# Kernel optimization log

Hardware: AMD Instinct MI355X
Metric: run time of the kernel (lower is better)

The kernel has to match this reference:

```python
import jax, jax.numpy as jnp
import numpy as np

B, S, D, H = 8, 2048, 1024, 64


def setup_inputs() -> dict:
    key = jax.random.key(0)
    ks = jax.random.split(key, 9)
    s = 0.02
    return {
        "x": jax.random.normal(ks[0], (B, S, D), jnp.float32),
        "Wq": jax.random.normal(ks[1], (H, D), jnp.float32) * s,
        "bq": jnp.zeros((H,), jnp.float32),
        "Wk": jax.random.normal(ks[2], (H, D), jnp.float32) * s,
        "bk": jnp.zeros((H,), jnp.float32),
        "Wv": jax.random.normal(ks[3], (H, D), jnp.float32) * s,
        "bv": jnp.zeros((H,), jnp.float32),
        "Wo": jax.random.normal(ks[4], (H, H), jnp.float32) * s,
        "bo": jnp.zeros((H,), jnp.float32),
    }


def reference(x, Wq, bq, Wk, bk, Wv, bv, Wo, bo):
    # Linear layers: y = x @ W.T + b (torch nn.Linear convention)
    q = jnp.einsum("bsd,hd->bsh", x, Wq) + bq  # [B,S,H]
    k = jnp.einsum("bsd,hd->bsh", x, Wk) + bk
    v = jnp.einsum("bsd,hd->bsh", x, Wv) + bv
    scale = jnp.float32(H) ** 0.5
    scores = jnp.einsum("bsh,bth->bst", q, k) / scale  # [B,S,S]
    causal = jnp.tril(jnp.ones((S, S), bool))
    scores = jnp.where(causal, scores, -jnp.inf)
    attn = jax.nn.softmax(scores, axis=-1)
    out = jnp.einsum("bst,bth->bsh", attn, v)  # [B,S,H]
    out = jnp.einsum("bsh,gh->bsg", out, Wo) + bo  # output proj [H,H]
    return out
```

## Files before the change

kernel.cpp:

```cpp
#include <hip/hip_runtime.h>
#include <hip/hip_bf16.h>

#define NB 8
#define NS 2048
#define ND 1024
#define NH 64
#define NM (NB*NS)

typedef __attribute__((ext_vector_type(8))) short short8;
typedef __attribute__((ext_vector_type(4))) short short4v;
typedef __attribute__((ext_vector_type(4))) float f32x4;
typedef __attribute__((ext_vector_type(4))) float f4;

#define QSCALE (0.125f * 1.44269504088896340736f)

__device__ __forceinline__ unsigned short f2bf(float f) {
    union { __hip_bfloat16 h; unsigned short u; } cv;
    cv.h = __float2bfloat16(f);
    return cv.u;
}

__global__ __launch_bounds__(256) void convw_kernel(
    const float* __restrict__ Wq, const float* __restrict__ bq,
    const float* __restrict__ Wk, const float* __restrict__ bk,
    const float* __restrict__ Wv, const float* __restrict__ bv,
    const float* __restrict__ Wo,
    unsigned short* __restrict__ Wb, unsigned short* __restrict__ Wob,
    float* __restrict__ biasb)
{
    const int row = blockIdx.x;
    const int t = threadIdx.x;
    if (row < 192) {
        const float* W = row < 64 ? Wq : (row < 128 ? Wk : Wv);
        const float sc = row < 64 ? QSCALE : 1.0f;
        f4 v = *(const f4*)&W[(size_t)(row & 63) * ND + t * 4];
        short4v o;
#pragma unroll
        for (int j = 0; j < 4; ++j) o[j] = (short)f2bf(v[j] * sc);
        *(short4v*)&Wb[(size_t)row * ND + t * 4] = o;
        if (row == 0 && t < 192) {
            const float* bsrc = t < 64 ? bq : (t < 128 ? bk : bv);
            biasb[t] = bsrc[t & 63] * (t < 64 ? QSCALE : 1.0f);
        }
    } else if (t < 16) {
        f4 v = *(const f4*)&Wo[(size_t)(row - 192) * 64 + t * 4];
        short4v o;
#pragma unroll
        for (int j = 0; j < 4; ++j) o[j] = (short)f2bf(v[j]);
        *(short4v*)&Wob[(size_t)(row - 192) * 64 + t * 4] = o;
    }
}

__global__ __launch_bounds__(512, 4) void qkv_kernel(
    const float* __restrict__ x, const unsigned short* __restrict__ Wb,
    const float* __restrict__ biasb,
    unsigned short* __restrict__ q, unsigned short* __restrict__ k,
    unsigned short* __restrict__ vT)
{
    __shared__ unsigned short As[2][32 * 64];
    __shared__ unsigned short Bs[2][192 * 64];

    const int t = threadIdx.x;
    const int lane = t & 63, g = lane >> 4, li = lane & 15;
    const int w = t >> 6, rg = w >> 2, cg = w & 3;
    const int m0 = blockIdx.x * 32;
    const int arow = t >> 4, ac = t & 15;

    f32x4 acc[3];
#pragma unroll
    for (int nf = 0; nf < 3; ++nf) acc[nf] = (f32x4)0.f;

    f4 xa[2]; short8 wr[2][3];

#define QKV_LOAD(KS, SL)                                                          \
    {                                                                             \
        xa[SL] = *(const f4*)&x[(size_t)(m0 + arow) * ND + (KS) * 64 + ac * 4];   \
        wr[SL][0] = *(const short8*)&Wb[(size_t)(t >> 3) * ND + (KS) * 64 + (t & 7) * 8];                  \
        wr[SL][1] = *(const short8*)&Wb[(size_t)((t + 512) >> 3) * ND + (KS) * 64 + ((t + 512) & 7) * 8];  \
        wr[SL][2] = *(const short8*)&Wb[(size_t)((t + 1024) >> 3) * ND + (KS) * 64 + ((t + 1024) & 7) * 8];\
    }

#define QKV_COMMIT(SL, BUF)                                                       \
    {                                                                             \
        short4v av_;                                                              \
        for (int j_ = 0; j_ < 4; ++j_) av_[j_] = (short)f2bf(xa[SL][j_]);         \
        *(short4v*)&As[BUF][arow * 64 + (((ac >> 1) ^ (arow & 7)) << 3) + (ac & 1) * 4] = av_; \
        int r0_ = t >> 3, c0_ = t & 7;                                            \
        *(short8*)&Bs[BUF][r0_ * 64 + ((c0_ ^ (r0_ & 7)) << 3)] = wr[SL][0];      \
        int r1_ = (t + 512) >> 3, c1_ = (t + 512) & 7;                            \
        *(short8*)&Bs[BUF][r1_ * 64 + ((c1_ ^ (r1_ & 7)) << 3)] = wr[SL][1];      \
        int r2_ = (t + 1024) >> 3, c2_ = (t + 1024) & 7;                          \
        *(short8*)&Bs[BUF][r2_ * 64 + ((c2_ ^ (r2_ & 7)) << 3)] = wr[SL][2];      \
    }

    QKV_LOAD(0, 0);
    QKV_LOAD(1, 1);
    QKV_COMMIT(0, 0);
    __syncthreads();

#pragma unroll
    for (int ks = 0; ks < 16; ++ks) {
        const int cur = ks & 1;
        if (ks < 14) QKV_LOAD(ks + 2, cur);
#pragma unroll
        for (int h = 0; h < 2; ++h) {
            short8 af = *(const short8*)&As[cur][(rg * 16 + li) * 64 + (((g + 4 * h) ^ (li & 7)) << 3)];
#pragma unroll
            for (int nf = 0; nf < 3; ++nf) {
                short8 bf = *(const short8*)&Bs[cur][(cg * 48 + nf * 16 + li) * 64 + (((g + 4 * h) ^ (li & 7)) << 3)];
                acc[nf] = __builtin_amdgcn_mfma_f32_16x16x32_bf16(af, bf, acc[nf], 0, 0, 0);
            }
        }
        if (ks < 15) QKV_COMMIT((ks + 1) & 1, cur ^ 1);
        __syncthreads();
    }

#pragma unroll
    for (int nf = 0; nf < 3; ++nf) {
        const int col = cg * 48 + nf * 16 + li;
        const float bias = biasb[col];
        const int row0 = m0 + rg * 16 + 4 * g;
        if (col < 64) {
#pragma unroll
            for (int i = 0; i < 4; ++i)
                q[(size_t)(row0 + i) * NH + col] = f2bf(acc[nf][i] + bias);
        } else if (col < 128) {
#pragma unroll
            for (int i = 0; i < 4; ++i)
                k[(size_t)(row0 + i) * NH + (col - 64)] = f2bf(acc[nf][i] + bias);
        } else {
            short4v pk;
#pragma unroll
            for (int i = 0; i < 4; ++i) pk[i] = (short)f2bf(acc[nf][i] + bias);
            const int bb = row0 >> 11, s = row0 & 2047;
            *(short4v*)&vT[(size_t)(bb * NH + (col - 128)) * NS + s] = pk;
        }
    }
}

__global__ __launch_bounds__(256, 2) void attn_kernel(
    const unsigned short* __restrict__ q, const unsigned short* __restrict__ k,
    const unsigned short* __restrict__ vT,
    float* __restrict__ Opart, float* __restrict__ lpart,
    int ctLog, int MAXC)
{
    __shared__ unsigned short Ks[2][64 * 64];
    __shared__ unsigned short Vs[2][64 * 64];
    __shared__ unsigned short Ps[4][16 * 64];

    const int t = threadIdx.x;
    const int w = t >> 6, lane = t & 63, g = lane >> 4, li = lane & 15;
    const int b = blockIdx.x & 7;
    const int pid = blockIdx.x >> 3;
    const int CT = 1 << ctLog;

    int qt = 0, c = 0;
    {
        int acc = 0;
        for (int u = 31; u >= 0; --u) {
            int nch = (u + CT) >> ctLog;
            if (pid < acc + nch) { qt = u; c = pid - acc; break; }
            acc += nch;
        }
    }
    const int t0 = c * CT;
    const int rem = qt + 1 - t0;
    const int tcount = rem < CT ? rem : CT;

    const size_t qkbase = (size_t)b * NS * NH;
    const int qrow = qt * 64 + w * 16 + li;
    const short8 qa0 = *(const short8*)&q[qkbase + (size_t)qrow * NH + g * 8];
    const short8 qa1 = *(const short8*)&q[qkbase + (size_t)qrow * NH + 32 + g * 8];

    float l_i[4]; f32x4 oacc[4];
#pragma unroll
    for (int i = 0; i < 4; ++i) { l_i[i] = 0.f; oacc[i] = (f32x4)0.f; }

    const int srow = t >> 3, sch = t & 7;
    short8 kreg0, kreg1, vreg0, vreg1;

    {
        const int kv0 = t0 * 64;
        kreg0 = *(const short8*)&k[qkbase + (size_t)(kv0 + srow) * NH + sch * 8];
        kreg1 = *(const short8*)&k[qkbase + (size_t)(kv0 + srow + 32) * NH + sch * 8];
        vreg0 = *(const short8*)&vT[(size_t)(b * NH + srow) * NS + kv0 + sch * 8];
        vreg1 = *(const short8*)&vT[(size_t)(b * NH + srow + 32) * NS + kv0 + sch * 8];
        *(short8*)&Ks[0][srow * 64 + ((sch ^ (srow & 7)) << 3)] = kreg0;
        *(short8*)&Ks[0][(srow + 32) * 64 + ((sch ^ (srow & 7)) << 3)] = kreg1;
        *(short8*)&Vs[0][srow * 64 + ((sch ^ (srow & 7)) << 3)] = vreg0;
        *(short8*)&Vs[0][(srow + 32) * 64 + ((sch ^ (srow & 7)) << 3)] = vreg1;
    }
    __syncthreads();

    for (int tt = 0; tt < tcount; ++tt) {
        const int cur = tt & 1;
        const int kv0 = (t0 + tt) * 64;
        if (tt + 1 < tcount) {
            const int nv0 = kv0 + 64;
            kreg0 = *(const short8*)&k[qkbase + (size_t)(nv0 + srow) * NH + sch * 8];
            kreg1 = *(const short8*)&k[qkbase + (size_t)(nv0 + srow + 32) * NH + sch * 8];
            vreg0 = *(const short8*)&vT[(size_t)(b * NH + srow) * NS + nv0 + sch * 8];
            vreg1 = *(const short8*)&vT[(size_t)(b * NH + srow + 32) * NS + nv0 + sch * 8];
        }
        f32x4 s[4];
#pragma unroll
        for (int c4 = 0; c4 < 4; ++c4) {
            s[c4] = (f32x4)0.f;
            const int krow = 16 * c4 + li;
            short8 kf0 = *(const short8*)&Ks[cur][krow * 64 + ((g ^ (li & 7)) << 3)];
            s[c4] = __builtin_amdgcn_mfma_f32_16x16x32_bf16(qa0, kf0, s[c4], 0, 0, 0);
            short8 kf1 = *(const short8*)&Ks[cur][krow * 64 + (((g + 4) ^ (li & 7)) << 3)];
            s[c4] = __builtin_amdgcn_mfma_f32_16x16x32_bf16(qa1, kf1, s[c4], 0, 0, 0);
        }
        if (kv0 == qt * 64) {
#pragma unroll
            for (int c4 = 0; c4 < 4; ++c4)
#pragma unroll
                for (int i = 0; i < 4; ++i)
                    if (16 * c4 + li > w * 16 + 4 * g + i) s[c4][i] = -1e30f;
        }
        float p[4][4];
#pragma unroll
        for (int c4 = 0; c4 < 4; ++c4)
#pragma unroll
            for (int i = 0; i < 4; ++i)
                p[c4][i] = exp2f(fminf(s[c4][i], 80.f));
#pragma unroll
        for (int i = 0; i < 4; ++i)
            l_i[i] += (p[0][i] + p[1][i]) + (p[2][i] + p[3][i]);

#pragma unroll
        for (int c4 = 0; c4 < 4; ++c4)
#pragma unroll
            for (int i = 0; i < 4; ++i) {
                const int prow = 4 * g + i;
                const int chunk = 2 * c4 + (li >> 3);
                Ps[w][prow * 64 + ((chunk ^ (prow & 7)) << 3) + (li & 7)] = f2bf(p[c4][i]);
            }
        short8 pf0 = *(const short8*)&Ps[w][li * 64 + ((g ^ (li & 7)) << 3)];
        short8 pf1 = *(const short8*)&Ps[w][li * 64 + (((g + 4) ^ (li & 7)) << 3)];
#pragma unroll
        for (int nf = 0; nf < 4; ++nf) {
            const int vrow = nf * 16 + li;
            short8 vf0 = *(const short8*)&Vs[cur][vrow * 64 + ((g ^ (li & 7)) << 3)];
            short8 vf1 = *(const short8*)&Vs[cur][vrow * 64 + (((g + 4) ^ (li & 7)) << 3)];
            oacc[nf] = __builtin_amdgcn_mfma_f32_16x16x32_bf16(pf0, vf0, oacc[nf], 0, 0, 0);
            oacc[nf] = __builtin_amdgcn_mfma_f32_16x16x32_bf16(pf1, vf1, oacc[nf], 0, 0, 0);
        }
        if (tt + 1 < tcount) {
            *(short8*)&Ks[cur ^ 1][srow * 64 + ((sch ^ (srow & 7)) << 3)] = kreg0;
            *(short8*)&Ks[cur ^ 1][(srow + 32) * 64 + ((sch ^ (srow & 7)) << 3)] = kreg1;
            *(short8*)&Vs[cur ^ 1][srow * 64 + ((sch ^ (srow & 7)) << 3)] = vreg0;
            *(short8*)&Vs[cur ^ 1][(srow + 32) * 64 + ((sch ^ (srow & 7)) << 3)] = vreg1;
        }
        __syncthreads();
    }

#pragma unroll
    for (int off = 1; off < 16; off <<= 1)
#pragma unroll
        for (int i = 0; i < 4; ++i) l_i[i] += __shfl_xor(l_i[i], off);

    const size_t slot = (size_t)((b * 32 + qt) * MAXC + c);
    float* Op = Opart + slot * 4096;
#pragma unroll
    for (int nf = 0; nf < 4; ++nf)
#pragma unroll
        for (int i = 0; i < 4; ++i)
            Op[(w * 16 + 4 * g + i) * 64 + nf * 16 + li] = oacc[nf][i];
    if (li == 0) {
#pragma unroll
        for (int i = 0; i < 4; ++i)
            lpart[slot * 64 + w * 16 + 4 * g + i] = l_i[i];
    }
}

__global__ __launch_bounds__(256, 2) void combine_kernel(
    const float* __restrict__ Opart, const float* __restrict__ lpart,
    const unsigned short* __restrict__ Wob, const float* __restrict__ bo,
    float* __restrict__ out, int ctLog, int MAXC)
{
    __shared__ unsigned short Osm[64 * 64];
    __shared__ float Linv[64];

    const int t = threadIdx.x;
    const int b = blockIdx.x & 7, qt = blockIdx.x >> 3;
    const int CT = 1 << ctLog;
    const int nch = (qt + CT) >> ctLog;
    const size_t base_slot = (size_t)(b * 32 + qt) * MAXC;

    if (t < 64) {
        float L = 0.f;
        for (int cc = 0; cc < nch; ++cc)
            L += lpart[(base_slot + cc) * 64 + t];
        Linv[t] = 1.f / L;
    }

    const int r = t >> 2, c0 = (t & 3) * 16;
    f4 a0 = (f4)0.f, a1 = (f4)0.f, a2 = (f4)0.f, a3 = (f4)0.f;
    for (int cc = 0; cc < nch; ++cc) {
        const float* P = Opart + (base_slot + cc) * 4096 + r * 64 + c0;
        a0 += *(const f4*)P; a1 += *(const f4*)(P + 4);
        a2 += *(const f4*)(P + 8); a3 += *(const f4*)(P + 12);
    }
    __syncthreads();
    {
        const float sc = Linv[r];
        short8 o0, o1;
#pragma unroll
        for (int j = 0; j < 4; ++j) {
            o0[j] = (short)f2bf(a0[j] * sc); o0[j + 4] = (short)f2bf(a1[j] * sc);
            o1[j] = (short)f2bf(a2[j] * sc); o1[j + 4] = (short)f2bf(a3[j] * sc);
        }
        const int ch0 = (t & 3) * 2;
        *(short8*)&Osm[r * 64 + ((ch0 ^ (r & 7)) << 3)] = o0;
        *(short8*)&Osm[r * 64 + (((ch0 + 1) ^ (r & 7)) << 3)] = o1;
    }
    __syncthreads();

    const int w = t >> 6, lane = t & 63, g = lane >> 4, li = lane & 15;
    f32x4 acc[4];
#pragma unroll
    for (int nf = 0; nf < 4; ++nf) acc[nf] = (f32x4)0.f;
#pragma unroll
    for (int s = 0; s < 2; ++s) {
        const int rr = w * 16 + li;
        short8 af = *(const short8*)&Osm[rr * 64 + (((g + 4 * s) ^ (rr & 7)) << 3)];
#pragma unroll
        for (int nf = 0; nf < 4; ++nf) {
            short8 bf = *(const short8*)&Wob[(size_t)(nf * 16 + li) * 64 + s * 32 + g * 8];
            acc[nf] = __builtin_amdgcn_mfma_f32_16x16x32_bf16(af, bf, acc[nf], 0, 0, 0);
        }
    }
#pragma unroll
    for (int nf = 0; nf < 4; ++nf) {
        const float bias = bo[nf * 16 + li];
#pragma unroll
        for (int i = 0; i < 4; ++i) {
            const size_t row = (size_t)b * NS + qt * 64 + w * 16 + 4 * g + i;
            out[row * 64 + nf * 16 + li] = acc[nf][i] + bias;
        }
    }
}

extern "C" void kernel_launch(void* const* d_in, const int* in_sizes, int n_in,
                              void* d_out, int out_size, void* d_ws, size_t ws_size,
                              hipStream_t stream)
{
    const float* x  = (const float*)d_in[0];
    const float* Wq = (const float*)d_in[1];
    const float* bq = (const float*)d_in[2];
    const float* Wk = (const float*)d_in[3];
    const float* bk = (const float*)d_in[4];
    const float* Wv = (const float*)d_in[5];
    const float* bv = (const float*)d_in[6];
    const float* Wo = (const float*)d_in[7];
    const float* bo = (const float*)d_in[8];
    float* out = (float*)d_out;

    size_t off = 0;
    auto alloc = [&](size_t bytes) {
        char* p = (char*)d_ws + off;
        off += (bytes + 255) & ~(size_t)255;
        return (void*)p;
    };
    unsigned short* qb  = (unsigned short*)alloc((size_t)NM * NH * 2);
    unsigned short* kb  = (unsigned short*)alloc((size_t)NM * NH * 2);
    unsigned short* vtb = (unsigned short*)alloc((size_t)NM * NH * 2);
    unsigned short* Wb  = (unsigned short*)alloc((size_t)192 * ND * 2);
    unsigned short* Wob = (unsigned short*)alloc((size_t)64 * 64 * 2);
    float* biasb = (float*)alloc(192 * 4);
    const size_t base = off;

    int ctLog = 5, MAXC = 1;
    const int cands[4] = {2, 3, 4, 5};
    for (int ci = 0; ci < 4; ++ci) {
        const int cl = cands[ci];
        const int mc = (31 >> cl) + 1;
        const size_t nslot = (size_t)256 * mc;
        const size_t need = base + nslot * (4096 + 64) * 4 + 8192;
        if (need <= ws_size) { ctLog = cl; MAXC = mc; break; }
    }
    const size_t NSLOT = (size_t)256 * MAXC;
    float* Opart = (float*)alloc(NSLOT * 4096 * 4);
    float* lpart = (float*)alloc(NSLOT * 64 * 4);

    const int CT = 1 << ctLog;
    int NCperB = 0;
    for (int qt = 0; qt < 32; ++qt) NCperB += (qt + CT) >> ctLog;

    convw_kernel<<<256, 256, 0, stream>>>(Wq, bq, Wk, bk, Wv, bv, Wo, Wb, Wob, biasb);
    qkv_kernel<<<NM / 32, 512, 0, stream>>>(x, Wb, biasb, qb, kb, vtb);
    attn_kernel<<<8 * NCperB, 256, 0, stream>>>(qb, kb, vtb, Opart, lpart, ctLog, MAXC);
    combine_kernel<<<256, 256, 0, stream>>>(Opart, lpart, Wob, bo, out, ctLog, MAXC);
}
```

Before: 52.22 us.

## Retile QKV projection into 64-row by 96-column blocks and drop smallest split-KV chunk

The QKV projection kernel now gives each block 64 rows of x and half of the 192 output columns, launching two blocks per 64-row tile. Each block stages a larger A tile and a smaller weight tile in LDS, using 8-wide bf16 stores. The aim is to cut weight traffic per output row and rebalance MFMA work across waves. The cost is that each x tile is now read by two blocks, which relies on adjacent blocks hitting in cache. The split-KV chunk search also no longer tries the smallest chunk size, so the attention kernel writes fewer partial results and the combine step has less to merge, at some cost in parallelism.

Result: slower. 57.07 us (+9.3%).

```diff
diff --git a/kernel.cpp b/kernel.cpp
--- a/kernel.cpp
+++ b/kernel.cpp
@@ -57,40 +57,47 @@
     unsigned short* __restrict__ q, unsigned short* __restrict__ k,
     unsigned short* __restrict__ vT)
 {
-    __shared__ unsigned short As[2][32 * 64];
-    __shared__ unsigned short Bs[2][192 * 64];
+    __shared__ unsigned short As[2][64 * 64];
+    __shared__ unsigned short Bs[2][96 * 64];
 
     const int t = threadIdx.x;
     const int lane = t & 63, g = lane >> 4, li = lane & 15;
-    const int w = t >> 6, rg = w >> 2, cg = w & 3;
-    const int m0 = blockIdx.x * 32;
-    const int arow = t >> 4, ac = t & 15;
+    const int w = t >> 6;
+    const int rgw = w >> 1, cgw = w & 1;
+    const int half = blockIdx.x & 1;
+    const int m0 = (blockIdx.x >> 1) * 64;
+    const int arow = t >> 3, ach = t & 7;
+    const int wrow0 = t >> 3;
+    const int wrow1 = 64 + (t >> 3);
+    const int wch = t & 7;
+    const bool hasB = (t < 256);
 
     f32x4 acc[3];
 #pragma unroll
     for (int nf = 0; nf < 3; ++nf) acc[nf] = (f32x4)0.f;
 
-    f4 xa[2]; short8 wr[2][3];
+    f4 xa[2][2]; short8 wr[2][2];
 
 #define QKV_LOAD(KS, SL)                                                          \
     {                                                                             \
-        xa[SL] = *(const f4*)&x[(size_t)(m0 + arow) * ND + (KS) * 64 + ac * 4];   \
-        wr[SL][0] = *(const short8*)&Wb[(size_t)(t >> 3) * ND + (KS) * 64 + (t & 7) * 8];                  \
-        wr[SL][1] = *(const short8*)&Wb[(size_t)((t + 512) >> 3) * ND + (KS) * 64 + ((t + 512) & 7) * 8];  \
-        wr[SL][2] = *(const short8*)&Wb[(size_t)((t + 1024) >> 3) * ND + (KS) * 64 + ((t + 1024) & 7) * 8];\
+        const float* p_ = &x[(size_t)(m0 + arow) * ND + (KS) * 64 + ach * 8];     \
+        xa[SL][0] = *(const f4*)p_; xa[SL][1] = *(const f4*)(p_ + 4);             \
+        wr[SL][0] = *(const short8*)&Wb[(size_t)(half * 96 + wrow0) * ND + (KS) * 64 + wch * 8]; \
+        if (hasB)                                                                 \
+            wr[SL][1] = *(const short8*)&Wb[(size_t)(half * 96 + wrow1) * ND + (KS) * 64 + wch * 8]; \
     }
 
 #define QKV_COMMIT(SL, BUF)                                                       \
     {                                                                             \
-        short4v av_;                                                              \
-        for (int j_ = 0; j_ < 4; ++j_) av_[j_] = (short)f2bf(xa[SL][j_]);         \
-        *(short4v*)&As[BUF][arow * 64 + (((ac >> 1) ^ (arow & 7)) << 3) + (ac & 1) * 4] = av_; \
-        int r0_ = t >> 3, c0_ = t & 7;                                            \
-        *(short8*)&Bs[BUF][r0_ * 64 + ((c0_ ^ (r0_ & 7)) << 3)] = wr[SL][0];      \
-        int r1_ = (t + 512) >> 3, c1_ = (t + 512) & 7;                            \
-        *(short8*)&Bs[BUF][r1_ * 64 + ((c1_ ^ (r1_ & 7)) << 3)] = wr[SL][1];      \
-        int r2_ = (t + 1024) >> 3, c2_ = (t + 1024) & 7;                          \
-        *(short8*)&Bs[BUF][r2_ * 64 + ((c2_ ^ (r2_ & 7)) << 3)] = wr[SL][2];      \
+        short8 av_;                                                               \
+        for (int j_ = 0; j_ < 4; ++j_) {                                          \
+            av_[j_] = (short)f2bf(xa[SL][0][j_]);                                 \
+            av_[j_ + 4] = (short)f2bf(xa[SL][1][j_]);                             \
+        }                                                                         \
+        *(short8*)&As[BUF][arow * 64 + ((ach ^ (arow & 7)) << 3)] = av_;          \
+        *(short8*)&Bs[BUF][wrow0 * 64 + ((wch ^ (wrow0 & 7)) << 3)] = wr[SL][0];  \
+        if (hasB)                                                                 \
+            *(short8*)&Bs[BUF][wrow1 * 64 + ((wch ^ (wrow1 & 7)) << 3)] = wr[SL][1]; \
     }
 
     QKV_LOAD(0, 0);
@@ -104,10 +111,10 @@
         if (ks < 14) QKV_LOAD(ks + 2, cur);
 #pragma unroll
         for (int h = 0; h < 2; ++h) {
-            short8 af = *(const short8*)&As[cur][(rg * 16 + li) * 64 + (((g + 4 * h) ^ (li & 7)) << 3)];
+            short8 af = *(const short8*)&As[cur][(rgw * 16 + li) * 64 + (((g + 4 * h) ^ (li & 7)) << 3)];
 #pragma unroll
             for (int nf = 0; nf < 3; ++nf) {
-                short8 bf = *(const short8*)&Bs[cur][(cg * 48 + nf * 16 + li) * 64 + (((g + 4 * h) ^ (li & 7)) << 3)];
+                short8 bf = *(const short8*)&Bs[cur][(cgw * 48 + nf * 16 + li) * 64 + (((g + 4 * h) ^ (li & 7)) << 3)];
                 acc[nf] = __builtin_amdgcn_mfma_f32_16x16x32_bf16(af, bf, acc[nf], 0, 0, 0);
             }
         }
@@ -117,9 +124,9 @@
 
 #pragma unroll
     for (int nf = 0; nf < 3; ++nf) {
-        const int col = cg * 48 + nf * 16 + li;
+        const int col = half * 96 + cgw * 48 + nf * 16 + li;
         const float bias = biasb[col];
-        const int row0 = m0 + rg * 16 + 4 * g;
+        const int row0 = m0 + rgw * 16 + 4 * g;
         if (col < 64) {
 #pragma unroll
             for (int i = 0; i < 4; ++i)
@@ -373,8 +380,8 @@
     const size_t base = off;
 
     int ctLog = 5, MAXC = 1;
-    const int cands[4] = {2, 3, 4, 5};
-    for (int ci = 0; ci < 4; ++ci) {
+    const int cands[3] = {3, 4, 5};
+    for (int ci = 0; ci < 3; ++ci) {
         const int cl = cands[ci];
         const int mc = (31 >> cl) + 1;
         const size_t nslot = (size_t)256 * mc;
@@ -390,7 +397,7 @@
     for (int qt = 0; qt < 32; ++qt) NCperB += (qt + CT) >> ctLog;
 
     convw_kernel<<<256, 256, 0, stream>>>(Wq, bq, Wk, bk, Wv, bv, Wo, Wb, Wob, biasb);
-    qkv_kernel<<<NM / 32, 512, 0, stream>>>(x, Wb, biasb, qb, kb, vtb);
+    qkv_kernel<<<2 * (NM / 64), 512, 0, stream>>>(x, Wb, biasb, qb, kb, vtb);
     attn_kernel<<<8 * NCperB, 256, 0, stream>>>(qb, kb, vtb, Opart, lpart, ctLog, MAXC);
     combine_kernel<<<256, 256, 0, stream>>>(Opart, lpart, Wob, bo, out, ctLog, MAXC);
 }
```
